# Performance work log

Hardware: AMD Instinct MI355X
Metric: run time of the kernel (lower is better)

The kernel has to match this reference:

```python
import jax, jax.numpy as jnp
import numpy as np

NUM_HEADS = 8
CHUNK = 64
TOP_K = 5


def setup_inputs() -> dict:
    key = jax.random.key(0)
    ks = jax.random.split(key, 5)
    D = 512
    x = jax.random.normal(ks[0], (1, 2048, D), dtype=jnp.float32)
    s = 0.02
    Wq = jax.random.normal(ks[1], (D, D), dtype=jnp.float32) * s
    Wk = jax.random.normal(ks[2], (D, D), dtype=jnp.float32) * s
    Wv = jax.random.normal(ks[3], (D, D), dtype=jnp.float32) * s
    Wo = jax.random.normal(ks[4], (D, D), dtype=jnp.float32) * s
    return {"x": x, "Wq": Wq, "Wk": Wk, "Wv": Wv, "Wo": Wo}


def reference(x, Wq, Wk, Wv, Wo):
    B, S, D = x.shape
    H = NUM_HEADS
    hd = D // H
    scale = hd ** -0.5
    C = S // CHUNK  # number of chunks

    def split_heads(t):
        return t.reshape(B, S, H, hd).transpose(0, 2, 1, 3)  # [B,H,S,hd]

    Q = split_heads(x @ Wq)
    K = split_heads(x @ Wk)
    V = split_heads(x @ Wv)

    # chunked K/V: [B,H,C,chunk,hd]
    Kc = K.reshape(B, H, C, CHUNK, hd)
    Vc = V.reshape(B, H, C, CHUNK, hd)

    # chunk descriptors: mean-pooled keys per chunk -> [B,H,C,hd]
    chunk_keys = Kc.mean(axis=3)

    # route each query to top-k chunks by scaled similarity
    sims = jnp.einsum('bhsd,bhcd->bhsc', Q, chunk_keys) * scale  # [B,H,S,C]
    _, idx = jax.lax.top_k(sims, TOP_K)  # [B,H,S,K]

    # gather selected K/V chunk blocks: [B,H,S,K,chunk,hd]
    idx_flat = idx.reshape(B, H, S * TOP_K)[:, :, :, None, None]
    Kg = jnp.take_along_axis(Kc, idx_flat, axis=2).reshape(B, H, S, TOP_K, CHUNK, hd)
    Vg = jnp.take_along_axis(Vc, idx_flat, axis=2).reshape(B, H, S, TOP_K, CHUNK, hd)

    # sparse block attention over the K*chunk gathered keys per query
    scores = jnp.einsum('bhsd,bhskcd->bhskc', Q, Kg) * scale
    attn = jax.nn.softmax(scores.reshape(B, H, S, TOP_K * CHUNK), axis=-1)
    attn = attn.reshape(B, H, S, TOP_K, CHUNK)
    out = jnp.einsum('bhskc,bhskcd->bhsd', attn, Vg)  # [B,H,S,hd]

    out = out.transpose(0, 2, 1, 3).reshape(B, S, D)
    return out @ Wo
```

## Files before the change

### kernel.cpp

```cpp
#include <hip/hip_runtime.h>
#include <hip/hip_bf16.h>
#include <math.h>

#define S_LEN 2048
#define D_DIM 512
#define H_NUM 8
#define HD    64
#define C_NUM 32
#define TOPK  5
#define SCALE 0.125f
#define QCAP  1024

typedef __attribute__((ext_vector_type(8))) short bf16x8;
typedef __attribute__((ext_vector_type(4))) float f32x4;
typedef __attribute__((ext_vector_type(4))) unsigned short us4;

__device__ __forceinline__ unsigned short f2b(float f) {
    __hip_bfloat16 h = __float2bfloat16(f);
    unsigned short u;
    __builtin_memcpy(&u, &h, 2);
    return u;
}
__device__ __forceinline__ bf16x8 pack8(float4 a, float4 b) {
    bf16x8 r;
    r[0] = (short)f2b(a.x); r[1] = (short)f2b(a.y);
    r[2] = (short)f2b(a.z); r[3] = (short)f2b(a.w);
    r[4] = (short)f2b(b.x); r[5] = (short)f2b(b.y);
    r[6] = (short)f2b(b.z); r[7] = (short)f2b(b.w);
    return r;
}
__device__ __forceinline__ float b2f(unsigned short u) {
    __hip_bfloat16 h;
    __builtin_memcpy(&h, &u, 2);
    return __bfloat162float(h);
}

#define BM 64
#define BN 64
#define BK 32

__device__ __forceinline__ void gemm_body(const float* __restrict__ A,
                                          const float* __restrict__ B,
                                          float* __restrict__ C,
                                          int M, int N, int K,
                                          int bx, int by) {
    __shared__ float As[BK][BM + 4];
    __shared__ float Bs[BK][BN];

    const int t  = threadIdx.x;
    const int tx = t & 15;
    const int ty = t >> 4;
    const int m0 = by * BM;
    const int n0 = bx * BN;

    float4 acc0 = make_float4(0.f,0.f,0.f,0.f);
    float4 acc1 = make_float4(0.f,0.f,0.f,0.f);
    float4 acc2 = make_float4(0.f,0.f,0.f,0.f);
    float4 acc3 = make_float4(0.f,0.f,0.f,0.f);

    const int ar = t >> 3;
    const int ac = (t & 7) * 4;
    const int br = t >> 4;
    const int bc = (t & 15) * 4;

    float4 a0, a1, b0, b1;
    auto LD = [&](int k0) {
        a0 = *(const float4*)&A[(size_t)(m0 + ar)      * K + k0 + ac];
        a1 = *(const float4*)&A[(size_t)(m0 + ar + 32) * K + k0 + ac];
        b0 = *(const float4*)&B[(size_t)(k0 + br)      * N + n0 + bc];
        b1 = *(const float4*)&B[(size_t)(k0 + br + 16) * N + n0 + bc];
    };

    LD(0);
    for (int k0 = 0; k0 < K; k0 += BK) {
        __syncthreads();
        As[ac+0][ar]    = a0.x; As[ac+1][ar]    = a0.y; As[ac+2][ar]    = a0.z; As[ac+3][ar]    = a0.w;
        As[ac+0][ar+32] = a1.x; As[ac+1][ar+32] = a1.y; As[ac+2][ar+32] = a1.z; As[ac+3][ar+32] = a1.w;
        *(float4*)&Bs[br][bc]      = b0;
        *(float4*)&Bs[br + 16][bc] = b1;
        __syncthreads();

        if (k0 + BK < K) LD(k0 + BK);

        #pragma unroll
        for (int kk = 0; kk < BK; ++kk) {
            float4 a = *(const float4*)&As[kk][ty * 4];
            float4 b = *(const float4*)&Bs[kk][tx * 4];
            acc0.x += a.x*b.x; acc0.y += a.x*b.y; acc0.z += a.x*b.z; acc0.w += a.x*b.w;
            acc1.x += a.y*b.x; acc1.y += a.y*b.y; acc1.z += a.y*b.z; acc1.w += a.y*b.w;
            acc2.x += a.z*b.x; acc2.y += a.z*b.y; acc2.z += a.z*b.z; acc2.w += a.z*b.w;
            acc3.x += a.w*b.x; acc3.y += a.w*b.y; acc3.z += a.w*b.z; acc3.w += a.w*b.w;
        }
    }

    *(float4*)&C[(size_t)(m0 + ty*4 + 0) * N + n0 + tx*4] = acc0;
    *(float4*)&C[(size_t)(m0 + ty*4 + 1) * N + n0 + tx*4] = acc1;
    *(float4*)&C[(size_t)(m0 + ty*4 + 2) * N + n0 + tx*4] = acc2;
    *(float4*)&C[(size_t)(m0 + ty*4 + 3) * N + n0 + tx*4] = acc3;
}

__global__ __launch_bounds__(256) void gemm_qkv(const float* __restrict__ A,
                                                const float* __restrict__ Wq,
                                                const float* __restrict__ Wk,
                                                float* __restrict__ Qb,
                                                float* __restrict__ Kb,
                                                unsigned short* __restrict__ xbf) {
    if (blockIdx.z == 0) {
        const int r0 = blockIdx.y * 64;
        const int c0 = blockIdx.x * 64;
        for (int i = threadIdx.x; i < 64 * 16; i += 256) {
            int r = i >> 4, c4 = (i & 15) * 4;
            float4 v = *(const float4*)&A[(size_t)(r0 + r) * D_DIM + c0 + c4];
            us4 o; o[0] = f2b(v.x); o[1] = f2b(v.y); o[2] = f2b(v.z); o[3] = f2b(v.w);
            *(us4*)&xbf[(size_t)(r0 + r) * D_DIM + c0 + c4] = o;
        }
    }
    const float* B = (blockIdx.z == 0) ? Wq : Wk;
    float*       C = (blockIdx.z == 0) ? Qb : Kb;
    gemm_body(A, B, C, S_LEN, D_DIM, D_DIM, blockIdx.x, blockIdx.y);
}

template <bool ABF16, bool CBF16>
__device__ __forceinline__ void gemm_bf16_body(const void* __restrict__ Aptr,
                                               const float* __restrict__ B,
                                               void* __restrict__ Cptr,
                                               int M, int N, int K,
                                               int bx, int by) {
    __shared__ unsigned short As[2][64][72];
    __shared__ unsigned short Bs[2][64][72];

    const int t  = threadIdx.x;
    const int m0 = by * 64;
    const int n0 = bx * 64;
    const int rl = t >> 2;
    const int c4 = (t & 3) * 16;

    const int lane = t & 63, w = t >> 6, lr = lane & 15, quad = lane >> 4;

    f32x4 acc[4] = {{0.f,0.f,0.f,0.f},{0.f,0.f,0.f,0.f},
                    {0.f,0.f,0.f,0.f},{0.f,0.f,0.f,0.f}};

    float4 fa[4]; bf16x8 ba[2]; float4 fb[4];
    auto LDA = [&](int k0) {
        if (ABF16) {
            const unsigned short* A = (const unsigned short*)Aptr;
            ba[0] = *(const bf16x8*)&A[(size_t)(m0 + rl) * K + k0 + c4];
            ba[1] = *(const bf16x8*)&A[(size_t)(m0 + rl) * K + k0 + c4 + 8];
        } else {
            const float* A = (const float*)Aptr;
            const float* p = &A[(size_t)(m0 + rl) * K + k0 + c4];
            fa[0] = *(const float4*)&p[0];  fa[1] = *(const float4*)&p[4];
            fa[2] = *(const float4*)&p[8];  fa[3] = *(const float4*)&p[12];
        }
    };
    auto LDB = [&](int k0) {
        const float* p = &B[(size_t)(k0 + rl) * N + n0 + c4];
        fb[0] = *(const float4*)&p[0];  fb[1] = *(const float4*)&p[4];
        fb[2] = *(const float4*)&p[8];  fb[3] = *(const float4*)&p[12];
    };
    auto STORE = [&](int pp) {
        if (ABF16) {
            *(bf16x8*)&As[pp][rl][c4]     = ba[0];
            *(bf16x8*)&As[pp][rl][c4 + 8] = ba[1];
        } else {
            *(bf16x8*)&As[pp][rl][c4]     = pack8(fa[0], fa[1]);
            *(bf16x8*)&As[pp][rl][c4 + 8] = pack8(fa[2], fa[3]);
        }
        #pragma unroll
        for (int f = 0; f < 4; ++f) {
            float4 v = fb[f];
            Bs[pp][c4 + f*4 + 0][rl] = f2b(v.x);
            Bs[pp][c4 + f*4 + 1][rl] = f2b(v.y);
            Bs[pp][c4 + f*4 + 2][rl] = f2b(v.z);
            Bs[pp][c4 + f*4 + 3][rl] = f2b(v.w);
        }
    };

    LDA(0); LDB(0);
    STORE(0);
    __syncthreads();

    int p = 0;
    for (int k0 = 0; k0 < K; k0 += 64) {
        const bool more = (k0 + 64 < K);
        if (more) { LDA(k0 + 64); LDB(k0 + 64); }

        bf16x8 a0 = *(const bf16x8*)&As[p][w * 16 + lr][quad * 8];
        bf16x8 a1 = *(const bf16x8*)&As[p][w * 16 + lr][32 + quad * 8];
        #pragma unroll
        for (int nt = 0; nt < 4; ++nt) {
            bf16x8 b0 = *(const bf16x8*)&Bs[p][nt * 16 + lr][quad * 8];
            bf16x8 b1 = *(const bf16x8*)&Bs[p][nt * 16 + lr][32 + quad * 8];
            acc[nt] = __builtin_amdgcn_mfma_f32_16x16x32_bf16(a0, b0, acc[nt], 0, 0, 0);
            acc[nt] = __builtin_amdgcn_mfma_f32_16x16x32_bf16(a1, b1, acc[nt], 0, 0, 0);
        }

        if (more) STORE(p ^ 1);
        __syncthreads();
        p ^= 1;
    }

    #pragma unroll
    for (int nt = 0; nt < 4; ++nt)
        #pragma unroll
        for (int r = 0; r < 4; ++r) {
            int m = m0 + w * 16 + quad * 4 + r;
            int n = n0 + nt * 16 + lr;
            if (CBF16) ((unsigned short*)Cptr)[(size_t)m * N + n] = f2b(acc[nt][r]);
            else       ((float*)Cptr)[(size_t)m * N + n] = acc[nt][r];
        }
}

__global__ __launch_bounds__(256) void gemm_v(const unsigned short* __restrict__ xbf,
                                              const float* __restrict__ Wv,
                                              unsigned short* __restrict__ Vbf,
                                              int* __restrict__ cur,
                                              const float* __restrict__ K,
                                              float* __restrict__ ck) {
    if (blockIdx.x == 8) {
        const int c = blockIdx.y;
        const int t = threadIdx.x;
        #pragma unroll
        for (int dd = 0; dd < 2; ++dd) {
            const int d = t + dd * 256;
            const float* p = K + (size_t)c * 64 * D_DIM + d;
            float sum = 0.f;
            #pragma unroll
            for (int r = 0; r < 64; ++r) sum += p[(size_t)r * D_DIM];
            ck[(size_t)c * D_DIM + d] = sum * (1.0f / 64.0f);
        }
        return;
    }
    if (blockIdx.x == 0 && blockIdx.y == 0) cur[threadIdx.x] = 0;
    gemm_bf16_body<true, true>(xbf, Wv, Vbf, S_LEN, D_DIM, D_DIM,
                               blockIdx.x, blockIdx.y);
}

__global__ __launch_bounds__(256) void gemm_out(const unsigned short* __restrict__ Obn,
                                                const float* __restrict__ Wo,
                                                float* __restrict__ out) {
    gemm_bf16_body<true, false>(Obn, Wo, out, S_LEN, D_DIM, D_DIM,
                                blockIdx.x, blockIdx.y);
}

__global__ __launch_bounds__(256) void sims_topk(const float* __restrict__ Q,
                                                 const float* __restrict__ ck,
                                                 int* __restrict__ cur,
                                                 unsigned short* __restrict__ qlist) {
    __shared__ float qtile[64][68];
    __shared__ float cks[32][68];
    __shared__ float simsb[64][36];
    __shared__ int   lds_cnt[32];
    __shared__ int   lds_base[32];

    const int t  = threadIdx.x;
    const int s0 = blockIdx.x * 64;
    const int h  = blockIdx.y;

    if (t < 32) lds_cnt[t] = 0;

    {
        int r = t >> 2;
        #pragma unroll
        for (int i = 0; i < 4; ++i) {
            int cf4 = (t & 3) * 4 + i;
            *(float4*)&qtile[r][cf4 * 4] =
                *(const float4*)&Q[(size_t)(s0 + r) * D_DIM + h * HD + cf4 * 4];
        }
    }
    for (int i = t; i < C_NUM * 16; i += 256) {
        int c = i >> 4, df4 = i & 15;
        *(float4*)&cks[c][df4 * 4] =
            *(const float4*)&ck[(size_t)c * D_DIM + h * HD + df4 * 4];
    }
    __syncthreads();

    {
        const int sl = t >> 2, g = t & 3;
        float sa[8] = {0.f,0.f,0.f,0.f,0.f,0.f,0.f,0.f};
        #pragma unroll
        for (int d4 = 0; d4 < 16; ++d4) {
            float4 q4 = *(const float4*)&qtile[sl][d4 * 4];
            #pragma unroll
            for (int j = 0; j < 8; ++j) {
                float4 c4 = *(const float4*)&cks[g * 8 + j][d4 * 4];
                sa[j] += q4.x*c4.x + q4.y*c4.y + q4.z*c4.z + q4.w*c4.w;
            }
        }
        *(float4*)&simsb[sl][g*8 + 0] = make_float4(sa[0], sa[1], sa[2], sa[3]);
        *(float4*)&simsb[sl][g*8 + 4] = make_float4(sa[4], sa[5], sa[6], sa[7]);
    }
    __syncthreads();

    int csel[TOPK], lpos[TOPK];
    if (t < 64) {
        float sv[32];
        #pragma unroll
        for (int cq = 0; cq < 8; ++cq) {
            float4 v = *(const float4*)&simsb[t][cq * 4];
            sv[cq*4+0] = v.x; sv[cq*4+1] = v.y; sv[cq*4+2] = v.z; sv[cq*4+3] = v.w;
        }
        #pragma unroll
        for (int k = 0; k < TOPK; ++k) {
            float best = -INFINITY; int bi = 0;
            #pragma unroll
            for (int cc = 0; cc < 32; ++cc) {
                bool gt = sv[cc] > best;
                best = gt ? sv[cc] : best;
                bi   = gt ? cc : bi;
            }
            #pragma unroll
            for (int cc = 0; cc < 32; ++cc)
                if (cc == bi) sv[cc] = -INFINITY;
            csel[k] = bi;
            lpos[k] = atomicAdd(&lds_cnt[bi], 1);
        }
    }
    __syncthreads();

    if (t < 32) lds_base[t] = atomicAdd(&cur[h * 32 + t], lds_cnt[t]);
    __syncthreads();

    if (t < 64) {
        #pragma unroll
        for (int k = 0; k < TOPK; ++k) {
            int c = csel[k];
            int pos = lds_base[c] + lpos[k];
            if (pos < QCAP)
                qlist[(size_t)(h * 32 + c) * QCAP + pos] =
                    (unsigned short)((s0 + t) | (k << 11));
        }
    }
}

__global__ __launch_bounds__(256) void moc_attn7(const float* __restrict__ Q,
                                                 const float* __restrict__ K,
                                                 const unsigned short* __restrict__ Vbf,
                                                 const int* __restrict__ cnt,
                                                 const unsigned short* __restrict__ qlist,
                                                 float* __restrict__ lpart,
                                                 float* __restrict__ Opart) {
    __shared__ unsigned short Qs[64][72];
    __shared__ unsigned short Ks[64][72];
    __shared__ unsigned short VT[64][72];
    __shared__ unsigned short Ps[64][72];
    __shared__ unsigned short slist[64];

    const int hc = blockIdx.y;
    const int h  = hc >> 5;
    const int c  = hc & 31;
    const int g0 = blockIdx.x;
    const int t  = threadIdx.x;

    const int count  = min(cnt[hc], QCAP);
    const int ntiles = (count + 63) >> 6;
    if (g0 >= ntiles) return;

    const float* Kb = K + ((size_t)c * 64) * D_DIM + h * HD;
    const unsigned short* Vb = Vbf + ((size_t)c * 64) * D_DIM + h * HD;

    const int j  = t >> 2;
    const int d0 = (t & 3) * 16;

    {
        const float* kr = Kb + (size_t)j * D_DIM + d0;
        float4 k0 = *(const float4*)&kr[0],  k1 = *(const float4*)&kr[4];
        float4 k2 = *(const float4*)&kr[8],  k3 = *(const float4*)&kr[12];
        *(bf16x8*)&Ks[j][d0]     = pack8(k0, k1);
        *(bf16x8*)&Ks[j][d0 + 8] = pack8(k2, k3);

        const unsigned short* vr = Vb + (size_t)j * D_DIM + d0;
        bf16x8 v0 = *(const bf16x8*)&vr[0];
        bf16x8 v1 = *(const bf16x8*)&vr[8];
        #pragma unroll
        for (int i = 0; i < 8; ++i) {
            VT[d0 + i][j]     = (unsigned short)v0[i];
            VT[d0 + 8 + i][j] = (unsigned short)v1[i];
        }
    }
    __syncthreads();

    const int lane = t & 63;
    const int w    = t >> 6;
    const int lr   = lane & 15;
    const int quad = lane >> 4;

    for (int ti = g0; ti < ntiles; ti += 2) {
        const int base = ti * 64;
        const int lim  = min(count - base, 64);
        const unsigned short* list = qlist + (size_t)hc * QCAP + base;

        {
            unsigned short pv = (j < lim) ? list[j] : (unsigned short)0xFFFF;
            if ((t & 3) == 0) slist[j] = pv;
            int s = (pv == 0xFFFF) ? 0 : (int)(pv & 2047);
            const float* qr = Q + (size_t)s * D_DIM + h * HD + d0;
            float4 q0 = *(const float4*)&qr[0],  q1 = *(const float4*)&qr[4];
            float4 q2 = *(const float4*)&qr[8],  q3 = *(const float4*)&qr[12];
            *(bf16x8*)&Qs[j][d0]     = pack8(q0, q1);
            *(bf16x8*)&Qs[j][d0 + 8] = pack8(q2, q3);
        }

        bf16x8 aq0 = *(const bf16x8*)&Qs[w * 16 + lr][quad * 8];
        bf16x8 aq1 = *(const bf16x8*)&Qs[w * 16 + lr][32 + quad * 8];

        f32x4 acc[4];
        #pragma unroll
        for (int kt = 0; kt < 4; ++kt) {
            bf16x8 b0 = *(const bf16x8*)&Ks[kt * 16 + lr][quad * 8];
            bf16x8 b1 = *(const bf16x8*)&Ks[kt * 16 + lr][32 + quad * 8];
            f32x4 z = {0.f, 0.f, 0.f, 0.f};
            z = __builtin_amdgcn_mfma_f32_16x16x32_bf16(aq0, b0, z, 0, 0, 0);
            z = __builtin_amdgcn_mfma_f32_16x16x32_bf16(aq1, b1, z, 0, 0, 0);
            acc[kt] = z;
        }

        unsigned short pb[4][4];
        float dsum[4] = {0.f, 0.f, 0.f, 0.f};
        #pragma unroll
        for (int kt = 0; kt < 4; ++kt) {
            #pragma unroll
            for (int r = 0; r < 4; ++r) {
                unsigned short u = f2b(__expf(acc[kt][r] * SCALE));
                pb[kt][r] = u;
                dsum[r] += b2f(u);
            }
        }
        #pragma unroll
        for (int r = 0; r < 4; ++r) {
            float v = dsum[r];
            v += __shfl_xor(v, 1, 64);
            v += __shfl_xor(v, 2, 64);
            v += __shfl_xor(v, 4, 64);
            v += __shfl_xor(v, 8, 64);
            dsum[r] = v;
        }
        if (lr == 0) {
            #pragma unroll
            for (int r = 0; r < 4; ++r) {
                unsigned short sv = slist[w * 16 + quad * 4 + r];
                if (sv != 0xFFFF) {
                    int kk = sv >> 11, s = sv & 2047;
                    lpart[((size_t)kk * H_NUM + h) * S_LEN + s] = dsum[r];
                }
            }
        }

        #pragma unroll
        for (int kt = 0; kt < 4; ++kt)
            #pragma unroll
            for (int r = 0; r < 4; ++r)
                Ps[w * 16 + quad * 4 + r][kt * 16 + lr] = pb[kt][r];

        bf16x8 ap0 = *(const bf16x8*)&Ps[w * 16 + lr][quad * 8];
        bf16x8 ap1 = *(const bf16x8*)&Ps[w * 16 + lr][32 + quad * 8];

        #pragma unroll
        for (int dt = 0; dt < 4; ++dt) {
            bf16x8 b0 = *(const bf16x8*)&VT[dt * 16 + lr][quad * 8];
            bf16x8 b1 = *(const bf16x8*)&VT[dt * 16 + lr][32 + quad * 8];
            f32x4 z = {0.f, 0.f, 0.f, 0.f};
            z = __builtin_amdgcn_mfma_f32_16x16x32_bf16(ap0, b0, z, 0, 0, 0);
            z = __builtin_amdgcn_mfma_f32_16x16x32_bf16(ap1, b1, z, 0, 0, 0);
            #pragma unroll
            for (int r = 0; r < 4; ++r) {
                unsigned short sv = slist[w * 16 + quad * 4 + r];
                if (sv != 0xFFFF) {
                    int kk = sv >> 11, s = sv & 2047;
                    Opart[((((size_t)kk * H_NUM + h) * S_LEN + s) * HD) + dt * 16 + lr] = z[r];
                }
            }
        }
    }
}

__global__ __launch_bounds__(256) void reduce_norm(const float4* __restrict__ Opart4,
                                                   const float* __restrict__ lpart,
                                                   unsigned short* __restrict__ Obn) {
    int i = blockIdx.x * 256 + threadIdx.x;
    int s    = i >> 7;
    int col4 = i & 127;
    int h    = col4 >> 4;
    int f4   = col4 & 15;
    float4 acc = make_float4(0.f,0.f,0.f,0.f);
    float  den = 0.f;
    #pragma unroll
    for (int k = 0; k < TOPK; ++k) {
        size_t slot = ((size_t)k * H_NUM + h) * S_LEN + s;
        float4 v = Opart4[slot * 16 + f4];
        acc.x += v.x; acc.y += v.y; acc.z += v.z; acc.w += v.w;
        den += lpart[slot];
    }
    float inv = 1.0f / den;
    us4 o;
    o[0] = f2b(acc.x * inv); o[1] = f2b(acc.y * inv);
    o[2] = f2b(acc.z * inv); o[3] = f2b(acc.w * inv);
    *(us4*)&Obn[(size_t)i * 4] = o;
}

extern "C" void kernel_launch(void* const* d_in, const int* in_sizes, int n_in,
                              void* d_out, int out_size, void* d_ws, size_t ws_size,
                              hipStream_t stream) {
    const float* x  = (const float*)d_in[0];
    const float* Wq = (const float*)d_in[1];
    const float* Wk = (const float*)d_in[2];
    const float* Wv = (const float*)d_in[3];
    const float* Wo = (const float*)d_in[4];
    float* out = (float*)d_out;

    const size_t SD = (size_t)S_LEN * D_DIM;
    float* ws    = (float*)d_ws;
    float* Qb    = ws;
    float* Kb    = Qb + SD;
    unsigned short* Vbf = (unsigned short*)(Kb + SD);
    float* ck    = (float*)(Vbf + SD);
    float* lpart = ck + (size_t)C_NUM * D_DIM;
    int*   curb  = (int*)(lpart + (size_t)TOPK * H_NUM * S_LEN);
    unsigned short* qlst = (unsigned short*)(curb + 256);
    float* Opart = (float*)(qlst + (size_t)256 * QCAP);
    unsigned short* xbf = (unsigned short*)(Opart + (size_t)TOPK * H_NUM * S_LEN * HD);
    unsigned short* Obn = (unsigned short*)Qb;

    dim3 qkgrid(D_DIM / BN, S_LEN / BM, 2);
    gemm_qkv<<<qkgrid, 256, 0, stream>>>(x, Wq, Wk, Qb, Kb, xbf);

    dim3 vgrid(D_DIM / 64 + 1, S_LEN / 64);
    gemm_v<<<vgrid, 256, 0, stream>>>(xbf, Wv, Vbf, curb, Kb, ck);

    dim3 rgrid(S_LEN / 64, H_NUM);
    sims_topk<<<rgrid, 256, 0, stream>>>(Qb, ck, curb, qlst);

    dim3 agrid(2, H_NUM * C_NUM);
    moc_attn7<<<agrid, 256, 0, stream>>>(Qb, Kb, Vbf, curb, qlst, lpart, Opart);

    reduce_norm<<<(int)(SD / 4 / 256), 256, 0, stream>>>((const float4*)Opart, lpart, Obn);

    dim3 ogrid(D_DIM / 64, S_LEN / 64);
    gemm_out<<<ogrid, 256, 0, stream>>>(Obn, Wo, out);
}
```

Before: 146.6 us.

## Fuse routing, attention, reduction and output GEMM into one cooperative kernel

Replaces the four trailing launches (sims/top-k, chunk attention, partial reduction, output projection) with one persistent cooperative kernel of 512 blocks. The phases are separated by grid-wide syncs, and the shared memory is a single buffer reinterpreted per phase. The top-k phase now splits each 64-query tile across two blocks so the work matches the fixed grid. This removes per-kernel launch gaps and tail effects, but adds three grid barriers and requires every block to be co-resident. The gemm_qkv body is also reordered so the bf16 conversion of x runs after the GEMM.

```diff
diff --git a/kernel.cpp b/kernel.cpp
--- a/kernel.cpp
+++ b/kernel.cpp
@@ -1,6 +1,9 @@
 #include <hip/hip_runtime.h>
 #include <hip/hip_bf16.h>
+#include <hip/hip_cooperative_groups.h>
 #include <math.h>
+
+namespace cg = cooperative_groups;
 
 #define S_LEN 2048
 #define D_DIM 512
@@ -105,6 +108,9 @@
                                                 float* __restrict__ Qb,
                                                 float* __restrict__ Kb,
                                                 unsigned short* __restrict__ xbf) {
+    const float* B = (blockIdx.z == 0) ? Wq : Wk;
+    float*       C = (blockIdx.z == 0) ? Qb : Kb;
+    gemm_body(A, B, C, S_LEN, D_DIM, D_DIM, blockIdx.x, blockIdx.y);
     if (blockIdx.z == 0) {
         const int r0 = blockIdx.y * 64;
         const int c0 = blockIdx.x * 64;
@@ -115,9 +121,6 @@
             *(us4*)&xbf[(size_t)(r0 + r) * D_DIM + c0 + c4] = o;
         }
     }
-    const float* B = (blockIdx.z == 0) ? Wq : Wk;
-    float*       C = (blockIdx.z == 0) ? Qb : Kb;
-    gemm_body(A, B, C, S_LEN, D_DIM, D_DIM, blockIdx.x, blockIdx.y);
 }
 
 template <bool ABF16, bool CBF16>
@@ -125,9 +128,10 @@
                                                const float* __restrict__ B,
                                                void* __restrict__ Cptr,
                                                int M, int N, int K,
-                                               int bx, int by) {
-    __shared__ unsigned short As[2][64][72];
-    __shared__ unsigned short Bs[2][64][72];
+                                               int bx, int by,
+                                               unsigned short* sm) {
+    auto As = (unsigned short (*)[64][72])sm;
+    auto Bs = (unsigned short (*)[64][72])(sm + 9216);
 
     const int t  = threadIdx.x;
     const int m0 = by * 64;
@@ -217,6 +221,7 @@
                                               int* __restrict__ cur,
                                               const float* __restrict__ K,
                                               float* __restrict__ ck) {
+    __shared__ unsigned short sm[18432];
     if (blockIdx.x == 8) {
         const int c = blockIdx.y;
         const int t = threadIdx.x;
@@ -233,269 +238,280 @@
     }
     if (blockIdx.x == 0 && blockIdx.y == 0) cur[threadIdx.x] = 0;
     gemm_bf16_body<true, true>(xbf, Wv, Vbf, S_LEN, D_DIM, D_DIM,
-                               blockIdx.x, blockIdx.y);
-}
-
-__global__ __launch_bounds__(256) void gemm_out(const unsigned short* __restrict__ Obn,
-                                                const float* __restrict__ Wo,
-                                                float* __restrict__ out) {
-    gemm_bf16_body<true, false>(Obn, Wo, out, S_LEN, D_DIM, D_DIM,
-                                blockIdx.x, blockIdx.y);
-}
-
-__global__ __launch_bounds__(256) void sims_topk(const float* __restrict__ Q,
-                                                 const float* __restrict__ ck,
-                                                 int* __restrict__ cur,
-                                                 unsigned short* __restrict__ qlist) {
-    __shared__ float qtile[64][68];
-    __shared__ float cks[32][68];
-    __shared__ float simsb[64][36];
-    __shared__ int   lds_cnt[32];
-    __shared__ int   lds_base[32];
-
-    const int t  = threadIdx.x;
-    const int s0 = blockIdx.x * 64;
-    const int h  = blockIdx.y;
-
-    if (t < 32) lds_cnt[t] = 0;
+                               blockIdx.x, blockIdx.y, sm);
+}
+
+__global__ __launch_bounds__(256, 2) void mega(const float* __restrict__ Q,
+                                               const float* __restrict__ ck,
+                                               int* __restrict__ cur,
+                                               unsigned short* __restrict__ qlist,
+                                               const float* __restrict__ K,
+                                               const unsigned short* __restrict__ Vbf,
+                                               float* __restrict__ lpart,
+                                               float* __restrict__ Opart,
+                                               unsigned short* __restrict__ Obn,
+                                               const float* __restrict__ Wo,
+                                               float* __restrict__ out) {
+    __shared__ __align__(16) char smem[37120];
+    cg::grid_group grid = cg::this_grid();
+
+    const int bid = blockIdx.x;
+    const int t   = threadIdx.x;
 
     {
-        int r = t >> 2;
+        const int half = bid & 1;
+        const int h    = (bid >> 1) & 7;
+        const int s0t  = bid >> 4;
+        const int sbase = s0t * 64 + half * 32;
+
+        auto qtile = (float (*)[68])(smem);
+        auto cks   = (float (*)[68])(smem + 8704);
+        auto simsb = (float (*)[36])(smem + 17408);
+        int* lds_cnt  = (int*)(smem + 22016);
+        int* lds_base = (int*)(smem + 22144);
+
+        if (t < 32) lds_cnt[t] = 0;
+
+        for (int i = t; i < 32 * 16; i += 256) {
+            int r = i >> 4, cf4 = i & 15;
+            *(float4*)&qtile[r][cf4 * 4] =
+                *(const float4*)&Q[(size_t)(sbase + r) * D_DIM + h * HD + cf4 * 4];
+        }
+        for (int i = t; i < C_NUM * 16; i += 256) {
+            int c = i >> 4, df4 = i & 15;
+            *(float4*)&cks[c][df4 * 4] =
+                *(const float4*)&ck[(size_t)c * D_DIM + h * HD + df4 * 4];
+        }
+        __syncthreads();
+
+        {
+            const int sl = t >> 3;
+            const int g  = t & 7;
+            float sa[4] = {0.f, 0.f, 0.f, 0.f};
+            #pragma unroll
+            for (int d4 = 0; d4 < 16; ++d4) {
+                float4 q4 = *(const float4*)&qtile[sl][d4 * 4];
+                #pragma unroll
+                for (int j = 0; j < 4; ++j) {
+                    float4 c4v = *(const float4*)&cks[g * 4 + j][d4 * 4];
+                    sa[j] += q4.x*c4v.x + q4.y*c4v.y + q4.z*c4v.z + q4.w*c4v.w;
+                }
+            }
+            *(float4*)&simsb[sl][g * 4] = make_float4(sa[0], sa[1], sa[2], sa[3]);
+        }
+        __syncthreads();
+
+        int csel[TOPK], lpos[TOPK];
+        if (t < 32) {
+            float sv[32];
+            #pragma unroll
+            for (int cq = 0; cq < 8; ++cq) {
+                float4 v = *(const float4*)&simsb[t][cq * 4];
+                sv[cq*4+0] = v.x; sv[cq*4+1] = v.y; sv[cq*4+2] = v.z; sv[cq*4+3] = v.w;
+            }
+            #pragma unroll
+            for (int k = 0; k < TOPK; ++k) {
+                float best = -INFINITY; int bi = 0;
+                #pragma unroll
+                for (int cc = 0; cc < 32; ++cc) {
+                    bool gt = sv[cc] > best;
+                    best = gt ? sv[cc] : best;
+                    bi   = gt ? cc : bi;
+                }
+                #pragma unroll
+                for (int cc = 0; cc < 32; ++cc)
+                    if (cc == bi) sv[cc] = -INFINITY;
+                csel[k] = bi;
+                lpos[k] = atomicAdd(&lds_cnt[bi], 1);
+            }
+        }
+        __syncthreads();
+
+        if (t < 32) lds_base[t] = atomicAdd(&cur[h * 32 + t], lds_cnt[t]);
+        __syncthreads();
+
+        if (t < 32) {
+            #pragma unroll
+            for (int k = 0; k < TOPK; ++k) {
+                int c = csel[k];
+                int pos = lds_base[c] + lpos[k];
+                if (pos < QCAP)
+                    qlist[(size_t)(h * 32 + c) * QCAP + pos] =
+                        (unsigned short)((sbase + t) | (k << 11));
+            }
+        }
+    }
+    grid.sync();
+
+    {
+        unsigned short* usm = (unsigned short*)smem;
+        auto Qs = (unsigned short (*)[72])(usm);
+        auto Ks = (unsigned short (*)[72])(usm + 4608);
+        auto VT = (unsigned short (*)[72])(usm + 9216);
+        auto Ps = (unsigned short (*)[72])(usm + 13824);
+        unsigned short* slist = usm + 18432;
+
+        const int hc = bid >> 1;
+        const int h  = hc >> 5;
+        const int c  = hc & 31;
+        const int g0 = bid & 1;
+
+        const int count  = min(cur[hc], QCAP);
+        const int ntiles = (count + 63) >> 6;
+
+        if (g0 < ntiles) {
+            const float* Kb = K + ((size_t)c * 64) * D_DIM + h * HD;
+            const unsigned short* Vb = Vbf + ((size_t)c * 64) * D_DIM + h * HD;
+
+            const int j  = t >> 2;
+            const int d0 = (t & 3) * 16;
+
+            {
+                const float* kr = Kb + (size_t)j * D_DIM + d0;
+                float4 k0 = *(const float4*)&kr[0],  k1 = *(const float4*)&kr[4];
+                float4 k2 = *(const float4*)&kr[8],  k3 = *(const float4*)&kr[12];
+                *(bf16x8*)&Ks[j][d0]     = pack8(k0, k1);
+                *(bf16x8*)&Ks[j][d0 + 8] = pack8(k2, k3);
+
+                const unsigned short* vr = Vb + (size_t)j * D_DIM + d0;
+                bf16x8 v0 = *(const bf16x8*)&vr[0];
+                bf16x8 v1 = *(const bf16x8*)&vr[8];
+                #pragma unroll
+                for (int i = 0; i < 8; ++i) {
+                    VT[d0 + i][j]     = (unsigned short)v0[i];
+                    VT[d0 + 8 + i][j] = (unsigned short)v1[i];
+                }
+            }
+            __syncthreads();
+
+            const int lane = t & 63;
+            const int w    = t >> 6;
+            const int lr   = lane & 15;
+            const int quad = lane >> 4;
+
+            for (int ti = g0; ti < ntiles; ti += 2) {
+                const int base = ti * 64;
+                const int lim  = min(count - base, 64);
+                const unsigned short* list = qlist + (size_t)hc * QCAP + base;
+
+                {
+                    unsigned short pv = (j < lim) ? list[j] : (unsigned short)0xFFFF;
+                    if ((t & 3) == 0) slist[j] = pv;
+                    int s = (pv == 0xFFFF) ? 0 : (int)(pv & 2047);
+                    const float* qr = Q + (size_t)s * D_DIM + h * HD + d0;
+                    float4 q0 = *(const float4*)&qr[0],  q1 = *(const float4*)&qr[4];
+                    float4 q2 = *(const float4*)&qr[8],  q3 = *(const float4*)&qr[12];
+                    *(bf16x8*)&Qs[j][d0]     = pack8(q0, q1);
+                    *(bf16x8*)&Qs[j][d0 + 8] = pack8(q2, q3);
+                }
+
+                bf16x8 aq0 = *(const bf16x8*)&Qs[w * 16 + lr][quad * 8];
+                bf16x8 aq1 = *(const bf16x8*)&Qs[w * 16 + lr][32 + quad * 8];
+
+                f32x4 acc[4];
+                #pragma unroll
+                for (int kt = 0; kt < 4; ++kt) {
+                    bf16x8 b0 = *(const bf16x8*)&Ks[kt * 16 + lr][quad * 8];
+                    bf16x8 b1 = *(const bf16x8*)&Ks[kt * 16 + lr][32 + quad * 8];
+                    f32x4 z = {0.f, 0.f, 0.f, 0.f};
+                    z = __builtin_amdgcn_mfma_f32_16x16x32_bf16(aq0, b0, z, 0, 0, 0);
+                    z = __builtin_amdgcn_mfma_f32_16x16x32_bf16(aq1, b1, z, 0, 0, 0);
+                    acc[kt] = z;
+                }
+
+                unsigned short pb[4][4];
+                float dsum[4] = {0.f, 0.f, 0.f, 0.f};
+                #pragma unroll
+                for (int kt = 0; kt < 4; ++kt) {
+                    #pragma unroll
+                    for (int r = 0; r < 4; ++r) {
+                        unsigned short u = f2b(__expf(acc[kt][r] * SCALE));
+                        pb[kt][r] = u;
+                        dsum[r] += b2f(u);
+                    }
+                }
+                #pragma unroll
+                for (int r = 0; r < 4; ++r) {
+                    float v = dsum[r];
+                    v += __shfl_xor(v, 1, 64);
+                    v += __shfl_xor(v, 2, 64);
+                    v += __shfl_xor(v, 4, 64);
+                    v += __shfl_xor(v, 8, 64);
+                    dsum[r] = v;
+                }
+                if (lr == 0) {
+                    #pragma unroll
+                    for (int r = 0; r < 4; ++r) {
+                        unsigned short sv = slist[w * 16 + quad * 4 + r];
+                        if (sv != 0xFFFF) {
+                            int kk = sv >> 11, s = sv & 2047;
+                            lpart[((size_t)kk * H_NUM + h) * S_LEN + s] = dsum[r];
+                        }
+                    }
+                }
+
+                #pragma unroll
+                for (int kt = 0; kt < 4; ++kt)
+                    #pragma unroll
+                    for (int r = 0; r < 4; ++r)
+                        Ps[w * 16 + quad * 4 + r][kt * 16 + lr] = pb[kt][r];
+
+                bf16x8 ap0 = *(const bf16x8*)&Ps[w * 16 + lr][quad * 8];
+                bf16x8 ap1 = *(const bf16x8*)&Ps[w * 16 + lr][32 + quad * 8];
+
+                #pragma unroll
+                for (int dt = 0; dt < 4; ++dt) {
+                    bf16x8 b0 = *(const bf16x8*)&VT[dt * 16 + lr][quad * 8];
+                    bf16x8 b1 = *(const bf16x8*)&VT[dt * 16 + lr][32 + quad * 8];
+                    f32x4 z = {0.f, 0.f, 0.f, 0.f};
+                    z = __builtin_amdgcn_mfma_f32_16x16x32_bf16(ap0, b0, z, 0, 0, 0);
+                    z = __builtin_amdgcn_mfma_f32_16x16x32_bf16(ap1, b1, z, 0, 0, 0);
+                    #pragma unroll
+                    for (int r = 0; r < 4; ++r) {
+                        unsigned short sv = slist[w * 16 + quad * 4 + r];
+                        if (sv != 0xFFFF) {
+                            int kk = sv >> 11, s = sv & 2047;
+                            Opart[((((size_t)kk * H_NUM + h) * S_LEN + s) * HD) + dt * 16 + lr] = z[r];
+                        }
+                    }
+                }
+            }
+        }
+    }
+    grid.sync();
+
+    {
+        const float4* Opart4 = (const float4*)Opart;
         #pragma unroll
-        for (int i = 0; i < 4; ++i) {
-            int cf4 = (t & 3) * 4 + i;
-            *(float4*)&qtile[r][cf4 * 4] =
-                *(const float4*)&Q[(size_t)(s0 + r) * D_DIM + h * HD + cf4 * 4];
-        }
-    }
-    for (int i = t; i < C_NUM * 16; i += 256) {
-        int c = i >> 4, df4 = i & 15;
-        *(float4*)&cks[c][df4 * 4] =
-            *(const float4*)&ck[(size_t)c * D_DIM + h * HD + df4 * 4];
-    }
-    __syncthreads();
-
-    {
-        const int sl = t >> 2, g = t & 3;
-        float sa[8] = {0.f,0.f,0.f,0.f,0.f,0.f,0.f,0.f};
-        #pragma unroll
-        for (int d4 = 0; d4 < 16; ++d4) {
-            float4 q4 = *(const float4*)&qtile[sl][d4 * 4];
+        for (int half = 0; half < 2; ++half) {
+            int i = bid * 512 + half * 256 + t;
+            int s    = i >> 7;
+            int col4 = i & 127;
+            int h    = col4 >> 4;
+            int f4   = col4 & 15;
+            float4 acc = make_float4(0.f,0.f,0.f,0.f);
+            float  den = 0.f;
             #pragma unroll
-            for (int j = 0; j < 8; ++j) {
-                float4 c4 = *(const float4*)&cks[g * 8 + j][d4 * 4];
-                sa[j] += q4.x*c4.x + q4.y*c4.y + q4.z*c4.z + q4.w*c4.w;
-            }
-        }
-        *(float4*)&simsb[sl][g*8 + 0] = make_float4(sa[0], sa[1], sa[2], sa[3]);
-        *(float4*)&simsb[sl][g*8 + 4] = make_float4(sa[4], sa[5], sa[6], sa[7]);
-    }
-    __syncthreads();
-
-    int csel[TOPK], lpos[TOPK];
-    if (t < 64) {
-        float sv[32];
-        #pragma unroll
-        for (int cq = 0; cq < 8; ++cq) {
-            float4 v = *(const float4*)&simsb[t][cq * 4];
-            sv[cq*4+0] = v.x; sv[cq*4+1] = v.y; sv[cq*4+2] = v.z; sv[cq*4+3] = v.w;
-        }
-        #pragma unroll
-        for (int k = 0; k < TOPK; ++k) {
-            float best = -INFINITY; int bi = 0;
-            #pragma unroll
-            for (int cc = 0; cc < 32; ++cc) {
-                bool gt = sv[cc] > best;
-                best = gt ? sv[cc] : best;
-                bi   = gt ? cc : bi;
-            }
-            #pragma unroll
-            for (int cc = 0; cc < 32; ++cc)
-                if (cc == bi) sv[cc] = -INFINITY;
-            csel[k] = bi;
-            lpos[k] = atomicAdd(&lds_cnt[bi], 1);
-        }
-    }
-    __syncthreads();
-
-    if (t < 32) lds_base[t] = atomicAdd(&cur[h * 32 + t], lds_cnt[t]);
-    __syncthreads();
-
-    if (t < 64) {
-        #pragma unroll
-        for (int k = 0; k < TOPK; ++k) {
-            int c = csel[k];
-            int pos = lds_base[c] + lpos[k];
-            if (pos < QCAP)
-                qlist[(size_t)(h * 32 + c) * QCAP + pos] =
-                    (unsigned short)((s0 + t) | (k << 11));
-        }
-    }
-}
-
-__global__ __launch_bounds__(256) void moc_attn7(const float* __restrict__ Q,
-                                                 const float* __restrict__ K,
-                                                 const unsigned short* __restrict__ Vbf,
-                                                 const int* __restrict__ cnt,
-                                                 const unsigned short* __restrict__ qlist,
-                                                 float* __restrict__ lpart,
-                                                 float* __restrict__ Opart) {
-    __shared__ unsigned short Qs[64][72];
-    __shared__ unsigned short Ks[64][72];
-    __shared__ unsigned short VT[64][72];
-    __shared__ unsigned short Ps[64][72];
-    __shared__ unsigned short slist[64];
-
-    const int hc = blockIdx.y;
-    const int h  = hc >> 5;
-    const int c  = hc & 31;
-    const int g0 = blockIdx.x;
-    const int t  = threadIdx.x;
-
-    const int count  = min(cnt[hc], QCAP);
-    const int ntiles = (count + 63) >> 6;
-    if (g0 >= ntiles) return;
-
-    const float* Kb = K + ((size_t)c * 64) * D_DIM + h * HD;
-    const unsigned short* Vb = Vbf + ((size_t)c * 64) * D_DIM + h * HD;
-
-    const int j  = t >> 2;
-    const int d0 = (t & 3) * 16;
-
-    {
-        const float* kr = Kb + (size_t)j * D_DIM + d0;
-        float4 k0 = *(const float4*)&kr[0],  k1 = *(const float4*)&kr[4];
-        float4 k2 = *(const float4*)&kr[8],  k3 = *(const float4*)&kr[12];
-        *(bf16x8*)&Ks[j][d0]     = pack8(k0, k1);
-        *(bf16x8*)&Ks[j][d0 + 8] = pack8(k2, k3);
-
-        const unsigned short* vr = Vb + (size_t)j * D_DIM + d0;
-        bf16x8 v0 = *(const bf16x8*)&vr[0];
-        bf16x8 v1 = *(const bf16x8*)&vr[8];
-        #pragma unroll
-        for (int i = 0; i < 8; ++i) {
-            VT[d0 + i][j]     = (unsigned short)v0[i];
-            VT[d0 + 8 + i][j] = (unsigned short)v1[i];
-        }
-    }
-    __syncthreads();
-
-    const int lane = t & 63;
-    const int w    = t >> 6;
-    const int lr   = lane & 15;
-    const int quad = lane >> 4;
-
-    for (int ti = g0; ti < ntiles; ti += 2) {
-        const int base = ti * 64;
-        const int lim  = min(count - base, 64);
-        const unsigned short* list = qlist + (size_t)hc * QCAP + base;
-
-        {
-            unsigned short pv = (j < lim) ? list[j] : (unsigned short)0xFFFF;
-            if ((t & 3) == 0) slist[j] = pv;
-            int s = (pv == 0xFFFF) ? 0 : (int)(pv & 2047);
-            const float* qr = Q + (size_t)s * D_DIM + h * HD + d0;
-            float4 q0 = *(const float4*)&qr[0],  q1 = *(const float4*)&qr[4];
-            float4 q2 = *(const float4*)&qr[8],  q3 = *(const float4*)&qr[12];
-            *(bf16x8*)&Qs[j][d0]     = pack8(q0, q1);
-            *(bf16x8*)&Qs[j][d0 + 8] = pack8(q2, q3);
-        }
-
-        bf16x8 aq0 = *(const bf16x8*)&Qs[w * 16 + lr][quad * 8];
-        bf16x8 aq1 = *(const bf16x8*)&Qs[w * 16 + lr][32 + quad * 8];
-
-        f32x4 acc[4];
-        #pragma unroll
-        for (int kt = 0; kt < 4; ++kt) {
-            bf16x8 b0 = *(const bf16x8*)&Ks[kt * 16 + lr][quad * 8];
-            bf16x8 b1 = *(const bf16x8*)&Ks[kt * 16 + lr][32 + quad * 8];
-            f32x4 z = {0.f, 0.f, 0.f, 0.f};
-            z = __builtin_amdgcn_mfma_f32_16x16x32_bf16(aq0, b0, z, 0, 0, 0);
-            z = __builtin_amdgcn_mfma_f32_16x16x32_bf16(aq1, b1, z, 0, 0, 0);
-            acc[kt] = z;
-        }
-
-        unsigned short pb[4][4];
-        float dsum[4] = {0.f, 0.f, 0.f, 0.f};
-        #pragma unroll
-        for (int kt = 0; kt < 4; ++kt) {
-            #pragma unroll
-            for (int r = 0; r < 4; ++r) {
-                unsigned short u = f2b(__expf(acc[kt][r] * SCALE));
-                pb[kt][r] = u;
-                dsum[r] += b2f(u);
-            }
-        }
-        #pragma unroll
-        for (int r = 0; r < 4; ++r) {
-            float v = dsum[r];
-            v += __shfl_xor(v, 1, 64);
-            v += __shfl_xor(v, 2, 64);
-            v += __shfl_xor(v, 4, 64);
-            v += __shfl_xor(v, 8, 64);
-            dsum[r] = v;
-        }
-        if (lr == 0) {
-            #pragma unroll
-            for (int r = 0; r < 4; ++r) {
-                unsigned short sv = slist[w * 16 + quad * 4 + r];
-                if (sv != 0xFFFF) {
-                    int kk = sv >> 11, s = sv & 2047;
-                    lpart[((size_t)kk * H_NUM + h) * S_LEN + s] = dsum[r];
-                }
-            }
-        }
-
-        #pragma unroll
-        for (int kt = 0; kt < 4; ++kt)
-            #pragma unroll
-            for (int r = 0; r < 4; ++r)
-                Ps[w * 16 + quad * 4 + r][kt * 16 + lr] = pb[kt][r];
-
-        bf16x8 ap0 = *(const bf16x8*)&Ps[w * 16 + lr][quad * 8];
-        bf16x8 ap1 = *(const bf16x8*)&Ps[w * 16 + lr][32 + quad * 8];
-
-        #pragma unroll
-        for (int dt = 0; dt < 4; ++dt) {
-            bf16x8 b0 = *(const bf16x8*)&VT[dt * 16 + lr][quad * 8];
-            bf16x8 b1 = *(const bf16x8*)&VT[dt * 16 + lr][32 + quad * 8];
-            f32x4 z = {0.f, 0.f, 0.f, 0.f};
-            z = __builtin_amdgcn_mfma_f32_16x16x32_bf16(ap0, b0, z, 0, 0, 0);
-            z = __builtin_amdgcn_mfma_f32_16x16x32_bf16(ap1, b1, z, 0, 0, 0);
-            #pragma unroll
-            for (int r = 0; r < 4; ++r) {
-                unsigned short sv = slist[w * 16 + quad * 4 + r];
-                if (sv != 0xFFFF) {
-                    int kk = sv >> 11, s = sv & 2047;
-                    Opart[((((size_t)kk * H_NUM + h) * S_LEN + s) * HD) + dt * 16 + lr] = z[r];
-                }
-            }
-        }
-    }
-}
-
-__global__ __launch_bounds__(256) void reduce_norm(const float4* __restrict__ Opart4,
-                                                   const float* __restrict__ lpart,
-                                                   unsigned short* __restrict__ Obn) {
-    int i = blockIdx.x * 256 + threadIdx.x;
-    int s    = i >> 7;
-    int col4 = i & 127;
-    int h    = col4 >> 4;
-    int f4   = col4 & 15;
-    float4 acc = make_float4(0.f,0.f,0.f,0.f);
-    float  den = 0.f;
-    #pragma unroll
-    for (int k = 0; k < TOPK; ++k) {
-        size_t slot = ((size_t)k * H_NUM + h) * S_LEN + s;
-        float4 v = Opart4[slot * 16 + f4];
-        acc.x += v.x; acc.y += v.y; acc.z += v.z; acc.w += v.w;
-        den += lpart[slot];
-    }
-    float inv = 1.0f / den;
-    us4 o;
-    o[0] = f2b(acc.x * inv); o[1] = f2b(acc.y * inv);
-    o[2] = f2b(acc.z * inv); o[3] = f2b(acc.w * inv);
-    *(us4*)&Obn[(size_t)i * 4] = o;
+            for (int k = 0; k < TOPK; ++k) {
+                size_t slot = ((size_t)k * H_NUM + h) * S_LEN + s;
+                float4 v = Opart4[slot * 16 + f4];
+                acc.x += v.x; acc.y += v.y; acc.z += v.z; acc.w += v.w;
+                den += lpart[slot];
+            }
+            float inv = 1.0f / den;
+            us4 o;
+            o[0] = f2b(acc.x * inv); o[1] = f2b(acc.y * inv);
+            o[2] = f2b(acc.z * inv); o[3] = f2b(acc.w * inv);
+            *(us4*)&Obn[(size_t)i * 4] = o;
+        }
+    }
+    grid.sync();
+
+    if (bid < 256) {
+        unsigned short* usm = (unsigned short*)smem;
+        gemm_bf16_body<true, false>(Obn, Wo, out, S_LEN, D_DIM, D_DIM,
+                                    bid & 7, bid >> 3, usm);
+    }
 }
 
 extern "C" void kernel_launch(void* const* d_in, const int* in_sizes, int n_in,
@@ -527,14 +543,11 @@
     dim3 vgrid(D_DIM / 64 + 1, S_LEN / 64);
     gemm_v<<<vgrid, 256, 0, stream>>>(xbf, Wv, Vbf, curb, Kb, ck);
 
-    dim3 rgrid(S_LEN / 64, H_NUM);
-    sims_topk<<<rgrid, 256, 0, stream>>>(Qb, ck, curb, qlst);
-
-    dim3 agrid(2, H_NUM * C_NUM);
-    moc_attn7<<<agrid, 256, 0, stream>>>(Qb, Kb, Vbf, curb, qlst, lpart, Opart);
-
-    reduce_norm<<<(int)(SD / 4 / 256), 256, 0, stream>>>((const float4*)Opart, lpart, Obn);
-
-    dim3 ogrid(D_DIM / 64, S_LEN / 64);
-    gemm_out<<<ogrid, 256, 0, stream>>>(Obn, Wo, out);
-}
+    void* margs[] = {
+        (void*)&Qb, (void*)&ck, (void*)&curb, (void*)&qlst,
+        (void*)&Kb, (void*)&Vbf, (void*)&lpart, (void*)&Opart,
+        (void*)&Obn, (void*)&Wo, (void*)&out
+    };
+    hipLaunchCooperativeKernel((void*)mega, dim3(512), dim3(256),
+                               margs, 0, stream);
+}
```

Measured after the change: 323.1 us. 120% more time.
